# Kernel optimization log

Hardware: AMD Instinct MI355X
Metric: run time of the kernel (lower is better)

The kernel has to match this reference:

```python
import jax, jax.numpy as jnp
from jax import lax
import numpy as np

B, T, D, H = 64, 512, 1024, 1024

def _lstm_layer(x_tbd, mask_tb, W, U, b):
    """Keras-style LSTM over time-major x (T,B,D). Gate order i,f,g,o.
    Masked timesteps carry previous h,c (Keras mask semantics)."""
    Bsz = x_tbd.shape[1]
    Hsz = U.shape[0]
    # precompute input projection once: (T,B,4H)
    xz = jnp.einsum('tbd,dh->tbh', x_tbd, W) + b

    def step(carry, inp):
        h, c = carry
        zx, m = inp
        z = zx + h @ U
        i, f, g, o = jnp.split(z, 4, axis=-1)
        i = jax.nn.sigmoid(i)
        f = jax.nn.sigmoid(f)
        g = jnp.tanh(g)
        o = jax.nn.sigmoid(o)
        c_new = f * c + i * g
        h_new = o * jnp.tanh(c_new)
        m = m[:, None]
        h2 = jnp.where(m, h_new, h)
        c2 = jnp.where(m, c_new, c)
        return (h2, c2), h2

    h0 = jnp.zeros((Bsz, Hsz), x_tbd.dtype)
    c0 = jnp.zeros((Bsz, Hsz), x_tbd.dtype)
    (h, c), hs = lax.scan(step, (h0, c0), (xz, mask_tb))
    return hs, h, c


def setup_inputs() -> dict:
    key = jax.random.key(0)
    ks = jax.random.split(key, 8)
    sD = 1.0 / np.sqrt(D)
    sH = 1.0 / np.sqrt(H)
    x = jax.random.normal(ks[0], (B, T, D), dtype=jnp.float32)
    lengths = jax.random.randint(ks[1], (B,), 1, T + 1, dtype=jnp.int32)
    # Keras unit_forget_bias: bias zeros except forget gate slice = 1
    b = jnp.zeros((4 * H,), jnp.float32).at[H:2 * H].set(1.0)
    return {
        'x': x,
        'lengths': lengths,
        'W0': jax.random.normal(ks[2], (D, 4 * H), dtype=jnp.float32) * sD,
        'U0': jax.random.normal(ks[3], (H, 4 * H), dtype=jnp.float32) * sH,
        'b0': b,
        'W1': jax.random.normal(ks[4], (H, 4 * H), dtype=jnp.float32) * sH,
        'U1': jax.random.normal(ks[5], (H, 4 * H), dtype=jnp.float32) * sH,
        'b1': b,
    }


def reference(x, lengths, W0, U0, b0, W1, U1, b1):
    Tlen = x.shape[1]
    mask = jnp.arange(Tlen)[None, :] < lengths[:, None]  # (B,T)
    mask_tb = mask.T  # (T,B)
    x_tbd = jnp.transpose(x, (1, 0, 2))  # time-major
    out0, _, _ = _lstm_layer(x_tbd, mask_tb, W0, U0, b0)
    out1, h, c = _lstm_layer(out0, mask_tb, W1, U1, b1)
    rnnout = jnp.transpose(out1, (1, 0, 2))  # (B,T,H)
    return rnnout, h, c
```

## Files before the change

kernel.cpp:

```cpp
#include <hip/hip_runtime.h>
#include <hip/hip_bf16.h>


#define NTT 512

typedef __attribute__((ext_vector_type(8))) short short8;
typedef __attribute__((ext_vector_type(4))) float floatx4;
typedef __attribute__((ext_vector_type(4))) unsigned short ushort4v;
typedef unsigned long long ull;

#define LDS_TOTAL 90112

#define AT_LD(p) __hip_atomic_load((p), __ATOMIC_RELAXED, __HIP_MEMORY_SCOPE_AGENT)
#define AT_ST(p, v) __hip_atomic_store((p), (v), __ATOMIC_RELAXED, __HIP_MEMORY_SCOPE_AGENT)
#define AT_ADD(p, v) __hip_atomic_fetch_add((p), (v), __ATOMIC_RELAXED, __HIP_MEMORY_SCOPE_AGENT)

__device__ __forceinline__ unsigned short f2bf(float f) {
  unsigned int u = __float_as_uint(f);
  u += 0x7fffu + ((u >> 16) & 1u);
  return (unsigned short)(u >> 16);
}
__device__ __forceinline__ float sigmf(float x) { return 1.0f / (1.0f + __expf(-x)); }
__device__ __forceinline__ float tanhfa(float x) { return 1.0f - 2.0f / (1.0f + __expf(2.0f * x)); }

__device__ __forceinline__ void fullbar(ull* fb) {
  __syncthreads();
  if (threadIdx.x == 0) {
    __builtin_amdgcn_fence(__ATOMIC_RELEASE, "agent");
    AT_ADD(fb, 1ull);
    while (AT_LD(fb) < 256ull) __builtin_amdgcn_s_sleep(1);
    __builtin_amdgcn_fence(__ATOMIC_ACQUIRE, "agent");
  }
  __syncthreads();
}

__device__ __forceinline__ void layer_arrive(ull* base, int sub) {
  asm volatile("s_waitcnt vmcnt(0)" ::: "memory");
  __syncthreads();
  if (threadIdx.x == 0) AT_ADD(base + 16 + 16 * (sub & 7), 1ull);
}

__device__ __forceinline__ ull leafmin(const ull* base) {
  ull v[8];
#pragma unroll
  for (int l = 0; l < 8; ++l) v[l] = AT_LD(base + 16 + 16 * l);
  ull m = v[0];
#pragma unroll
  for (int l = 1; l < 8; ++l) m = v[l] < m ? v[l] : m;
  return m;
}

__device__ __forceinline__ void wait2(const ull* own, long long ot, const ull* oth, long long xt) {
  if (threadIdx.x == 0) {
    if (ot > 0) {
      const ull tgt = 16ull * (ull)ot;
      while (leafmin(own) < tgt) __builtin_amdgcn_s_sleep(1);
    }
    if (xt > 0) {
      const ull tgt = 16ull * (ull)xt;
      while (leafmin(oth) < tgt) __builtin_amdgcn_s_sleep(1);
    }
    __builtin_amdgcn_fence(__ATOMIC_ACQUIRE, "agent");
  }
  __syncthreads();
}

__device__ __forceinline__ short8 ldfrag(const char* p) { return *(const short8*)p; }

__device__ __forceinline__ void ringfill(const char* const* aPm, short8 (*af)[4]) {
#pragma unroll
  for (int kt = 0; kt < 8; ++kt)
#pragma unroll
    for (int mt = 0; mt < 4; ++mt) af[kt][mt] = ldfrag(aPm[mt] + kt * 64);
}

__device__ __forceinline__ void kmain(const char* const* aPm, short8 (*af)[4],
                                      const short8 (*bfr)[2], floatx4 (*acc)[2]) {
#pragma unroll
  for (int kt = 0; kt < 16; ++kt) {
#pragma unroll
    for (int mt = 0; mt < 4; ++mt)
#pragma unroll
      for (int nt = 0; nt < 2; ++nt)
        acc[mt][nt] = __builtin_amdgcn_mfma_f32_16x16x32_bf16(
            af[kt & 7][mt], bfr[kt][nt], acc[mt][nt], 0, 0, 0);
    if (kt < 8) {
#pragma unroll
      for (int mt = 0; mt < 4; ++mt)
        af[kt & 7][mt] = ldfrag(aPm[mt] + (kt + 8) * 64);
    }
  }
}

__global__ __launch_bounds__(256, 1) void lstm2_persist(
    const float* __restrict__ xin, const int* __restrict__ lens,
    const float* __restrict__ W0, const float* __restrict__ U0, const float* __restrict__ b0v,
    const float* __restrict__ W1, const float* __restrict__ U1, const float* __restrict__ b1v,
    float* __restrict__ out, ull* __restrict__ ws) {
  extern __shared__ char smem[];
  float* red = (float*)smem;

  ull* bar0 = ws;
  ull* bar1 = ws + 512;
  ull* fbar = ws + 1024;
  unsigned short* hbufs = (unsigned short*)(ws + 2048);

  const int tid = threadIdx.x;
  const int bid = blockIdx.x;
  const int layer = bid >> 7;
  const int sub = bid & 127;
  const int hc0 = sub * 8;
  const int wave = tid >> 6;
  const int lane = tid & 63;
  const int c16 = lane & 15;
  const int rowgrp = lane >> 4;

  unsigned short* h0r[4] = {hbufs, hbufs + 65536, hbufs + 131072, hbufs + 196608};
  unsigned short* h1r[2] = {hbufs + 262144, hbufs + 327680};

  const unsigned int gid = (unsigned int)bid * 256u + (unsigned int)tid;
  for (unsigned int i = gid; i < 196608u; i += 65536u) ((unsigned int*)hbufs)[i] = 0u;
  {
    const floatx4* xs = (const floatx4*)xin;
    for (unsigned int q = gid; q < 8388608u; q += 65536u) {
      unsigned int d4 = q & 255u;
      unsigned int bt = q >> 8;
      floatx4 v = xs[q];
      ushort4v o;
      o.x = f2bf(v.x); o.y = f2bf(v.y); o.z = f2bf(v.z); o.w = f2bf(v.w);
      *((ushort4v*)((char*)out + (size_t)bt * 4096) + d4) = o;
    }
  }
  const float* Wm = layer ? W1 : W0;
  const float* Um = layer ? U1 : U0;
  const float* Bsrc = (wave < 2) ? Wm : Um;
  const int kbase = (wave & 1) * 512;
  short8 bf[16][2];
#pragma unroll
  for (int kt = 0; kt < 16; ++kt)
#pragma unroll
    for (int nt = 0; nt < 2; ++nt) {
      const int zc = (nt * 2 + (c16 >> 3)) * 1024 + hc0 + (c16 & 7);
      const float* col = Bsrc + (size_t)(kbase + kt * 32 + rowgrp * 8) * 4096 + zc;
      short8 v;
#pragma unroll
      for (int j = 0; j < 8; ++j) v[j] = (short)f2bf(col[(size_t)j * 4096]);
      bf[kt][nt] = v;
    }
  const float* bv = layer ? b1v : b0v;
  const float bias0 = bv[(c16 >> 3) * 1024 + hc0 + (c16 & 7)];
  const float bias1 = bv[(2 + (c16 >> 3)) * 1024 + hc0 + (c16 & 7)];
  int lens4[4];
#pragma unroll
  for (int r = 0; r < 4; ++r) lens4[r] = lens[wave * 16 + rowgrp * 4 + r];

  fullbar(fbar);

  float hst[4] = {0.f, 0.f, 0.f, 0.f};
  float cst[4] = {0.f, 0.f, 0.f, 0.f};
  const int col = hc0 + c16;

#pragma unroll 1
  for (int t = 0; t < NTT; ++t) {
    const char* aPm[4];
    short8 af[8][4];
    bool isX;
    {
      const char* base0;
      size_t pitch;
      if (layer == 0) {
        if (wave < 2) { base0 = (const char*)out + (size_t)t * 4096 + (size_t)wave * 1024;
                        pitch = (size_t)NTT * 4096; isX = true; }
        else          { base0 = (const char*)h0r[(t + 3) & 3] + (size_t)(wave - 2) * 1024;
                        pitch = 2048; isX = false; }
      } else {
        if (wave < 2) { base0 = (const char*)h0r[t & 3] + (size_t)wave * 1024; }
        else          { base0 = (const char*)h1r[(t + 1) & 1] + (size_t)(wave - 2) * 1024; }
        pitch = 2048; isX = false;
      }
      const char* aP = base0 + (size_t)c16 * pitch + (size_t)rowgrp * 16;
#pragma unroll
      for (int mt = 0; mt < 4; ++mt) aPm[mt] = aP + (size_t)mt * 16 * pitch;
    }

    if (isX) ringfill(aPm, af);

    if (layer == 0) wait2(bar0, t, bar1, (long long)t - 3);
    else            wait2(bar1, t, bar0, (long long)t + 1);

    floatx4 acc[4][2];
#pragma unroll
    for (int mt = 0; mt < 4; ++mt)
#pragma unroll
      for (int nt = 0; nt < 2; ++nt) { floatx4 z = {0.f, 0.f, 0.f, 0.f}; acc[mt][nt] = z; }

    if (isX) {
      kmain(aPm, af, bf, acc);
    } else {
      ringfill(aPm, af);
      kmain(aPm, af, bf, acc);
    }

#pragma unroll
    for (int mt = 0; mt < 4; ++mt)
      if (mt != wave) {
        int slot = mt * 3 + wave - (wave > mt ? 1 : 0);
        *(floatx4*)&red[((slot * 2 + 0) * 64 + lane) * 4] = acc[mt][0];
        *(floatx4*)&red[((slot * 2 + 1) * 64 + lane) * 4] = acc[mt][1];
      }
    __syncthreads();
    floatx4 z0 = acc[wave][0], z1 = acc[wave][1];
#pragma unroll
    for (int q = 0; q < 3; ++q) {
      int slot = wave * 3 + q;
      z0 += *(const floatx4*)&red[((slot * 2 + 0) * 64 + lane) * 4];
      z1 += *(const floatx4*)&red[((slot * 2 + 1) * 64 + lane) * 4];
    }
    z0 += bias0;
    z1 += bias1;

    unsigned short* hW = layer ? h1r[t & 1] : h0r[t & 3];
    float2 f2s[4];

#pragma unroll
    for (int r = 0; r < 4; ++r) {
      float zi = z0[r], zg = z1[r];
      float zf = __shfl_xor(zi, 8);
      float zo = __shfl_xor(zg, 8);
      float h2, hu_f = 0.f;
      unsigned short hu = 0;
      if (c16 < 8) {
        float ig = sigmf(zi), fg = sigmf(zf), gg = tanhfa(zg), og = sigmf(zo);
        float cn = fg * cst[r] + ig * gg;
        float hn = og * tanhfa(cn);
        bool m = t < lens4[r];
        h2 = m ? hn : hst[r];
        float c2 = m ? cn : cst[r];
        hst[r] = h2;
        cst[r] = c2;
        hu = f2bf(h2);
        hu_f = h2;
      }
      unsigned int up = __shfl_xor((unsigned int)hu, 1);
      float hp = __shfl_xor(hu_f, 1);
      if (c16 < 8 && !(c16 & 1)) {
        int b = wave * 16 + rowgrp * 4 + r;
        unsigned int w = (unsigned int)hu | (up << 16);
        AT_ST((unsigned int*)(hW + b * 1024 + col), w);
        f2s[r] = make_float2(hu_f, hp);
      }
    }

    if (layer == 0) layer_arrive(bar0, sub);
    else            layer_arrive(bar1, sub);

    if (layer && c16 < 8 && !(c16 & 1)) {
#pragma unroll
      for (int r = 0; r < 4; ++r) {
        int b = wave * 16 + rowgrp * 4 + r;
        *(float2*)&out[((size_t)b * 512 + (size_t)t) * 1024 + col] = f2s[r];
      }
    }
  }

  if (layer && c16 < 8) {
#pragma unroll
    for (int r = 0; r < 4; ++r) {
      int b = wave * 16 + rowgrp * 4 + r;
      out[(size_t)33554432 + (size_t)b * 1024 + col] = hst[r];
      out[(size_t)33554432 + 65536 + (size_t)b * 1024 + col] = cst[r];
    }
  }
}

extern "C" void kernel_launch(void* const* d_in, const int* in_sizes, int n_in,
                              void* d_out, int out_size, void* d_ws, size_t ws_size,
                              hipStream_t stream) {
  (void)in_sizes; (void)n_in; (void)out_size; (void)ws_size;
  const float* x  = (const float*)d_in[0];
  const int* lens = (const int*)d_in[1];
  const float* W0 = (const float*)d_in[2];
  const float* U0 = (const float*)d_in[3];
  const float* b0 = (const float*)d_in[4];
  const float* W1 = (const float*)d_in[5];
  const float* U1 = (const float*)d_in[6];
  const float* b1 = (const float*)d_in[7];

  (void)hipFuncSetAttribute((const void*)lstm2_persist,
                            hipFuncAttributeMaxDynamicSharedMemorySize, LDS_TOTAL);
  hipMemsetAsync(d_ws, 0, 16384, stream);

  lstm2_persist<<<dim3(256), dim3(256), LDS_TOTAL, stream>>>(
      x, lens, W0, U0, b0, W1, U1, b1, (float*)d_out, (ull*)d_ws);
}
```

Measured before the change: 9.748 ms.

## Halve persistent grid to 128 blocks, each computing 16 hidden columns

The persistent two-layer LSTM kernel now launches 128 blocks instead of 256, with each block owning 16 hidden units instead of 8. That doubles the register-resident weight fragments and the MFMA accumulators per block, and the A-fragment ring is shrunk from 8 to 4 k-steps to make room. The aim is to halve the number of participants in the per-timestep cross-block barriers and reuse each loaded h/x fragment across twice as many MFMAs. The costs are higher register pressure (possible spills), twice the serial MFMA work per block on each step, and only half of the CUs in use.

```diff
diff --git a/kernel.cpp b/kernel.cpp
--- a/kernel.cpp
+++ b/kernel.cpp
@@ -28,7 +28,7 @@
   if (threadIdx.x == 0) {
     __builtin_amdgcn_fence(__ATOMIC_RELEASE, "agent");
     AT_ADD(fb, 1ull);
-    while (AT_LD(fb) < 256ull) __builtin_amdgcn_s_sleep(1);
+    while (AT_LD(fb) < 128ull) __builtin_amdgcn_s_sleep(1);
     __builtin_amdgcn_fence(__ATOMIC_ACQUIRE, "agent");
   }
   __syncthreads();
@@ -53,11 +53,11 @@
 __device__ __forceinline__ void wait2(const ull* own, long long ot, const ull* oth, long long xt) {
   if (threadIdx.x == 0) {
     if (ot > 0) {
-      const ull tgt = 16ull * (ull)ot;
+      const ull tgt = 8ull * (ull)ot;
       while (leafmin(own) < tgt) __builtin_amdgcn_s_sleep(1);
     }
     if (xt > 0) {
-      const ull tgt = 16ull * (ull)xt;
+      const ull tgt = 8ull * (ull)xt;
       while (leafmin(oth) < tgt) __builtin_amdgcn_s_sleep(1);
     }
     __builtin_amdgcn_fence(__ATOMIC_ACQUIRE, "agent");
@@ -69,25 +69,25 @@
 
 __device__ __forceinline__ void ringfill(const char* const* aPm, short8 (*af)[4]) {
 #pragma unroll
-  for (int kt = 0; kt < 8; ++kt)
+  for (int kt = 0; kt < 4; ++kt)
 #pragma unroll
     for (int mt = 0; mt < 4; ++mt) af[kt][mt] = ldfrag(aPm[mt] + kt * 64);
 }
 
 __device__ __forceinline__ void kmain(const char* const* aPm, short8 (*af)[4],
-                                      const short8 (*bfr)[2], floatx4 (*acc)[2]) {
+                                      const short8 (*bfr)[4], floatx4 (*acc)[4]) {
 #pragma unroll
   for (int kt = 0; kt < 16; ++kt) {
 #pragma unroll
     for (int mt = 0; mt < 4; ++mt)
 #pragma unroll
-      for (int nt = 0; nt < 2; ++nt)
+      for (int nt = 0; nt < 4; ++nt)
         acc[mt][nt] = __builtin_amdgcn_mfma_f32_16x16x32_bf16(
-            af[kt & 7][mt], bfr[kt][nt], acc[mt][nt], 0, 0, 0);
-    if (kt < 8) {
+            af[kt & 3][mt], bfr[kt][nt], acc[mt][nt], 0, 0, 0);
+    if (kt < 12) {
 #pragma unroll
       for (int mt = 0; mt < 4; ++mt)
-        af[kt & 7][mt] = ldfrag(aPm[mt] + (kt + 8) * 64);
+        af[kt & 3][mt] = ldfrag(aPm[mt] + (kt + 4) * 64);
     }
   }
 }
@@ -107,9 +107,9 @@
 
   const int tid = threadIdx.x;
   const int bid = blockIdx.x;
-  const int layer = bid >> 7;
-  const int sub = bid & 127;
-  const int hc0 = sub * 8;
+  const int layer = bid >> 6;
+  const int sub = bid & 63;
+  const int hc0 = sub * 16;
   const int wave = tid >> 6;
   const int lane = tid & 63;
   const int c16 = lane & 15;
@@ -119,10 +119,10 @@
   unsigned short* h1r[2] = {hbufs + 262144, hbufs + 327680};
 
   const unsigned int gid = (unsigned int)bid * 256u + (unsigned int)tid;
-  for (unsigned int i = gid; i < 196608u; i += 65536u) ((unsigned int*)hbufs)[i] = 0u;
+  for (unsigned int i = gid; i < 196608u; i += 32768u) ((unsigned int*)hbufs)[i] = 0u;
   {
     const floatx4* xs = (const floatx4*)xin;
-    for (unsigned int q = gid; q < 8388608u; q += 65536u) {
+    for (unsigned int q = gid; q < 8388608u; q += 32768u) {
       unsigned int d4 = q & 255u;
       unsigned int bt = q >> 8;
       floatx4 v = xs[q];
@@ -135,12 +135,12 @@
   const float* Um = layer ? U1 : U0;
   const float* Bsrc = (wave < 2) ? Wm : Um;
   const int kbase = (wave & 1) * 512;
-  short8 bf[16][2];
+  short8 bf[16][4];
 #pragma unroll
   for (int kt = 0; kt < 16; ++kt)
 #pragma unroll
-    for (int nt = 0; nt < 2; ++nt) {
-      const int zc = (nt * 2 + (c16 >> 3)) * 1024 + hc0 + (c16 & 7);
+    for (int nt = 0; nt < 4; ++nt) {
+      const int zc = ((nt & 1) * 2 + (c16 >> 3)) * 1024 + hc0 + (nt >> 1) * 8 + (c16 & 7);
       const float* col = Bsrc + (size_t)(kbase + kt * 32 + rowgrp * 8) * 4096 + zc;
       short8 v;
 #pragma unroll
@@ -148,22 +148,25 @@
       bf[kt][nt] = v;
     }
   const float* bv = layer ? b1v : b0v;
-  const float bias0 = bv[(c16 >> 3) * 1024 + hc0 + (c16 & 7)];
-  const float bias1 = bv[(2 + (c16 >> 3)) * 1024 + hc0 + (c16 & 7)];
+  float bias0[2], bias1[2];
+#pragma unroll
+  for (int ch = 0; ch < 2; ++ch) {
+    bias0[ch] = bv[(c16 >> 3) * 1024 + hc0 + ch * 8 + (c16 & 7)];
+    bias1[ch] = bv[(2 + (c16 >> 3)) * 1024 + hc0 + ch * 8 + (c16 & 7)];
+  }
   int lens4[4];
 #pragma unroll
   for (int r = 0; r < 4; ++r) lens4[r] = lens[wave * 16 + rowgrp * 4 + r];
 
   fullbar(fbar);
 
-  float hst[4] = {0.f, 0.f, 0.f, 0.f};
-  float cst[4] = {0.f, 0.f, 0.f, 0.f};
-  const int col = hc0 + c16;
+  float hst[2][4] = {{0.f, 0.f, 0.f, 0.f}, {0.f, 0.f, 0.f, 0.f}};
+  float cst[2][4] = {{0.f, 0.f, 0.f, 0.f}, {0.f, 0.f, 0.f, 0.f}};
 
 #pragma unroll 1
   for (int t = 0; t < NTT; ++t) {
     const char* aPm[4];
-    short8 af[8][4];
+    short8 af[4][4];
     bool isX;
     {
       const char* base0;
@@ -188,11 +191,11 @@
     if (layer == 0) wait2(bar0, t, bar1, (long long)t - 3);
     else            wait2(bar1, t, bar0, (long long)t + 1);
 
-    floatx4 acc[4][2];
+    floatx4 acc[4][4];
 #pragma unroll
     for (int mt = 0; mt < 4; ++mt)
 #pragma unroll
-      for (int nt = 0; nt < 2; ++nt) { floatx4 z = {0.f, 0.f, 0.f, 0.f}; acc[mt][nt] = z; }
+      for (int nt = 0; nt < 4; ++nt) { floatx4 z = {0.f, 0.f, 0.f, 0.f}; acc[mt][nt] = z; }
 
     if (isX) {
       kmain(aPm, af, bf, acc);
@@ -205,49 +208,60 @@
     for (int mt = 0; mt < 4; ++mt)
       if (mt != wave) {
         int slot = mt * 3 + wave - (wave > mt ? 1 : 0);
-        *(floatx4*)&red[((slot * 2 + 0) * 64 + lane) * 4] = acc[mt][0];
-        *(floatx4*)&red[((slot * 2 + 1) * 64 + lane) * 4] = acc[mt][1];
+#pragma unroll
+        for (int nt = 0; nt < 4; ++nt)
+          *(floatx4*)&red[((slot * 4 + nt) * 64 + lane) * 4] = acc[mt][nt];
       }
     __syncthreads();
-    floatx4 z0 = acc[wave][0], z1 = acc[wave][1];
+    floatx4 z[4];
+#pragma unroll
+    for (int nt = 0; nt < 4; ++nt) z[nt] = acc[wave][nt];
 #pragma unroll
     for (int q = 0; q < 3; ++q) {
       int slot = wave * 3 + q;
-      z0 += *(const floatx4*)&red[((slot * 2 + 0) * 64 + lane) * 4];
-      z1 += *(const floatx4*)&red[((slot * 2 + 1) * 64 + lane) * 4];
-    }
-    z0 += bias0;
-    z1 += bias1;
+#pragma unroll
+      for (int nt = 0; nt < 4; ++nt)
+        z[nt] += *(const floatx4*)&red[((slot * 4 + nt) * 64 + lane) * 4];
+    }
+#pragma unroll
+    for (int ch = 0; ch < 2; ++ch) {
+      z[ch * 2 + 0] += bias0[ch];
+      z[ch * 2 + 1] += bias1[ch];
+    }
 
     unsigned short* hW = layer ? h1r[t & 1] : h0r[t & 3];
-    float2 f2s[4];
-
-#pragma unroll
-    for (int r = 0; r < 4; ++r) {
-      float zi = z0[r], zg = z1[r];
-      float zf = __shfl_xor(zi, 8);
-      float zo = __shfl_xor(zg, 8);
-      float h2, hu_f = 0.f;
-      unsigned short hu = 0;
-      if (c16 < 8) {
-        float ig = sigmf(zi), fg = sigmf(zf), gg = tanhfa(zg), og = sigmf(zo);
-        float cn = fg * cst[r] + ig * gg;
-        float hn = og * tanhfa(cn);
-        bool m = t < lens4[r];
-        h2 = m ? hn : hst[r];
-        float c2 = m ? cn : cst[r];
-        hst[r] = h2;
-        cst[r] = c2;
-        hu = f2bf(h2);
-        hu_f = h2;
-      }
-      unsigned int up = __shfl_xor((unsigned int)hu, 1);
-      float hp = __shfl_xor(hu_f, 1);
-      if (c16 < 8 && !(c16 & 1)) {
-        int b = wave * 16 + rowgrp * 4 + r;
-        unsigned int w = (unsigned int)hu | (up << 16);
-        AT_ST((unsigned int*)(hW + b * 1024 + col), w);
-        f2s[r] = make_float2(hu_f, hp);
+    float2 f2s[2][4];
+
+#pragma unroll
+    for (int ch = 0; ch < 2; ++ch) {
+      const int col = hc0 + ch * 8 + c16;
+#pragma unroll
+      for (int r = 0; r < 4; ++r) {
+        float zi = z[ch * 2 + 0][r], zg = z[ch * 2 + 1][r];
+        float zf = __shfl_xor(zi, 8);
+        float zo = __shfl_xor(zg, 8);
+        float h2, hu_f = 0.f;
+        unsigned short hu = 0;
+        if (c16 < 8) {
+          float ig = sigmf(zi), fg = sigmf(zf), gg = tanhfa(zg), og = sigmf(zo);
+          float cn = fg * cst[ch][r] + ig * gg;
+          float hn = og * tanhfa(cn);
+          bool m = t < lens4[r];
+          h2 = m ? hn : hst[ch][r];
+          float c2 = m ? cn : cst[ch][r];
+          hst[ch][r] = h2;
+          cst[ch][r] = c2;
+          hu = f2bf(h2);
+          hu_f = h2;
+        }
+        unsigned int up = __shfl_xor((unsigned int)hu, 1);
+        float hp = __shfl_xor(hu_f, 1);
+        if (c16 < 8 && !(c16 & 1)) {
+          int b = wave * 16 + rowgrp * 4 + r;
+          unsigned int w = (unsigned int)hu | (up << 16);
+          AT_ST((unsigned int*)(hW + b * 1024 + col), w);
+          f2s[ch][r] = make_float2(hu_f, hp);
+        }
       }
     }
 
@@ -256,19 +270,27 @@
 
     if (layer && c16 < 8 && !(c16 & 1)) {
 #pragma unroll
+      for (int ch = 0; ch < 2; ++ch) {
+        const int col = hc0 + ch * 8 + c16;
+#pragma unroll
+        for (int r = 0; r < 4; ++r) {
+          int b = wave * 16 + rowgrp * 4 + r;
+          *(float2*)&out[((size_t)b * 512 + (size_t)t) * 1024 + col] = f2s[ch][r];
+        }
+      }
+    }
+  }
+
+  if (layer && c16 < 8) {
+#pragma unroll
+    for (int ch = 0; ch < 2; ++ch) {
+      const int col = hc0 + ch * 8 + c16;
+#pragma unroll
       for (int r = 0; r < 4; ++r) {
         int b = wave * 16 + rowgrp * 4 + r;
-        *(float2*)&out[((size_t)b * 512 + (size_t)t) * 1024 + col] = f2s[r];
-      }
-    }
-  }
-
-  if (layer && c16 < 8) {
-#pragma unroll
-    for (int r = 0; r < 4; ++r) {
-      int b = wave * 16 + rowgrp * 4 + r;
-      out[(size_t)33554432 + (size_t)b * 1024 + col] = hst[r];
-      out[(size_t)33554432 + 65536 + (size_t)b * 1024 + col] = cst[r];
+        out[(size_t)33554432 + (size_t)b * 1024 + col] = hst[ch][r];
+        out[(size_t)33554432 + 65536 + (size_t)b * 1024 + col] = cst[ch][r];
+      }
     }
   }
 }
@@ -290,6 +312,6 @@
                             hipFuncAttributeMaxDynamicSharedMemorySize, LDS_TOTAL);
   hipMemsetAsync(d_ws, 0, 16384, stream);
 
-  lstm2_persist<<<dim3(256), dim3(256), LDS_TOTAL, stream>>>(
+  lstm2_persist<<<dim3(128), dim3(256), LDS_TOTAL, stream>>>(
       x, lens, W0, U0, b0, W1, U1, b1, (float*)d_out, (ull*)d_ws);
 }
```

Result: slower. 21.41 ms (+119.6%).

## Replace tree-counter barriers with per-block step flags and chunked waits

Applied to the files above, without the earlier changes.

Replaces the leaf-counter barrier (atomic adds plus a min over 8 leaves, waited on by thread 0 and then a block sync) with one flag word per producer block holding its latest timestep. Each wave polls only the 64 producer flags for the h slice it reads, using ballot. It then loads and computes in 4-chunk K slices as soon as each group of 16 producers is ready, overlapping the MFMA work with late producers. This cuts barrier latency and serialization on the recurrent critical path. The cost is more polling traffic, and the wait now relies on per-flag release ordering: there is no explicit acquire fence, only relaxed atomic loads.

```diff
diff --git a/kernel.cpp b/kernel.cpp
--- a/kernel.cpp
+++ b/kernel.cpp
@@ -34,38 +34,13 @@
   __syncthreads();
 }
 
-__device__ __forceinline__ void layer_arrive(ull* base, int sub) {
-  asm volatile("s_waitcnt vmcnt(0)" ::: "memory");
-  __syncthreads();
-  if (threadIdx.x == 0) AT_ADD(base + 16 + 16 * (sub & 7), 1ull);
-}
-
-__device__ __forceinline__ ull leafmin(const ull* base) {
-  ull v[8];
-#pragma unroll
-  for (int l = 0; l < 8; ++l) v[l] = AT_LD(base + 16 + 16 * l);
-  ull m = v[0];
-#pragma unroll
-  for (int l = 1; l < 8; ++l) m = v[l] < m ? v[l] : m;
-  return m;
-}
-
-__device__ __forceinline__ void wait2(const ull* own, long long ot, const ull* oth, long long xt) {
-  if (threadIdx.x == 0) {
-    if (ot > 0) {
-      const ull tgt = 16ull * (ull)ot;
-      while (leafmin(own) < tgt) __builtin_amdgcn_s_sleep(1);
-    }
-    if (xt > 0) {
-      const ull tgt = 16ull * (ull)xt;
-      while (leafmin(oth) < tgt) __builtin_amdgcn_s_sleep(1);
-    }
-    __builtin_amdgcn_fence(__ATOMIC_ACQUIRE, "agent");
-  }
-  __syncthreads();
-}
-
 __device__ __forceinline__ short8 ldfrag(const char* p) { return *(const short8*)p; }
+__device__ __forceinline__ short8 ldcoh(const char* p) {
+  union { short8 s; ull q[2]; } u;
+  u.q[0] = AT_LD((const ull*)p);
+  u.q[1] = AT_LD((const ull*)(p + 8));
+  return u.s;
+}
 
 __device__ __forceinline__ void ringfill(const char* const* aPm, short8 (*af)[4]) {
 #pragma unroll
@@ -90,6 +65,25 @@
         af[kt & 7][mt] = ldfrag(aPm[mt] + (kt + 8) * 64);
     }
   }
+}
+
+__device__ __forceinline__ void ringchunk(const char* const* aPm, short8 (*afc)[4], int kb) {
+#pragma unroll
+  for (int j = 0; j < 4; ++j)
+#pragma unroll
+    for (int mt = 0; mt < 4; ++mt) afc[j][mt] = ldcoh(aPm[mt] + (kb + j) * 64);
+}
+
+__device__ __forceinline__ void kchunk(const short8 (*afc)[4], const short8 (*bfr)[2],
+                                       floatx4 (*acc)[2], int kb) {
+#pragma unroll
+  for (int j = 0; j < 4; ++j)
+#pragma unroll
+    for (int mt = 0; mt < 4; ++mt)
+#pragma unroll
+      for (int nt = 0; nt < 2; ++nt)
+        acc[mt][nt] = __builtin_amdgcn_mfma_f32_16x16x32_bf16(
+            afc[j][mt], bfr[kb + j][nt], acc[mt][nt], 0, 0, 0);
 }
 
 __global__ __launch_bounds__(256, 1) void lstm2_persist(
@@ -100,8 +94,8 @@
   extern __shared__ char smem[];
   float* red = (float*)smem;
 
-  ull* bar0 = ws;
-  ull* bar1 = ws + 512;
+  unsigned* flags0 = (unsigned*)(ws + 16);
+  unsigned* flags1 = (unsigned*)(ws + 80);
   ull* fbar = ws + 1024;
   unsigned short* hbufs = (unsigned short*)(ws + 2048);
 
@@ -114,6 +108,7 @@
   const int lane = tid & 63;
   const int c16 = lane & 15;
   const int rowgrp = lane >> 4;
+  unsigned* flagsL = layer ? flags1 : flags0;
 
   unsigned short* h0r[4] = {hbufs, hbufs + 65536, hbufs + 131072, hbufs + 196608};
   unsigned short* h1r[2] = {hbufs + 262144, hbufs + 327680};
@@ -183,11 +178,6 @@
       for (int mt = 0; mt < 4; ++mt) aPm[mt] = aP + (size_t)mt * 16 * pitch;
     }
 
-    if (isX) ringfill(aPm, af);
-
-    if (layer == 0) wait2(bar0, t, bar1, (long long)t - 3);
-    else            wait2(bar1, t, bar0, (long long)t + 1);
-
     floatx4 acc[4][2];
 #pragma unroll
     for (int mt = 0; mt < 4; ++mt)
@@ -195,10 +185,37 @@
       for (int nt = 0; nt < 2; ++nt) { floatx4 z = {0.f, 0.f, 0.f, 0.f}; acc[mt][nt] = z; }
 
     if (isX) {
+      ringfill(aPm, af);
       kmain(aPm, af, bf, acc);
     } else {
-      ringfill(aPm, af);
-      kmain(aPm, af, bf, acc);
+      if (layer == 0 && t >= 4) {
+        const unsigned g4 = (unsigned)(t - 3);
+        while (true) {
+          bool ok = (AT_LD(flags1 + lane) >= g4) && (AT_LD(flags1 + 64 + lane) >= g4);
+          if (__all(ok)) break;
+          __builtin_amdgcn_s_sleep(2);
+        }
+      }
+      const unsigned* fl;
+      int half;
+      unsigned tgt;
+      if (layer == 0)      { fl = flags0; half = wave - 2; tgt = (unsigned)t; }
+      else if (wave < 2)   { fl = flags0; half = wave;     tgt = (unsigned)(t + 1); }
+      else                 { fl = flags1; half = wave - 2; tgt = (unsigned)t; }
+      const unsigned* fb = fl + half * 64;
+
+      ull rdy = __ballot(AT_LD(fb + lane) >= tgt);
+#pragma unroll
+      for (int g = 0; g < 4; ++g) {
+        const ull need = 0xFFFFull << (16 * g);
+        while ((rdy & need) != need) {
+          __builtin_amdgcn_s_sleep(1);
+          rdy = __ballot(AT_LD(fb + lane) >= tgt);
+        }
+        ringchunk(aPm, &af[(g & 1) * 4], g * 4);
+        if (g) kchunk(&af[((g - 1) & 1) * 4], bf, acc, (g - 1) * 4);
+      }
+      kchunk(&af[4], bf, acc, 12);
     }
 
 #pragma unroll
@@ -251,8 +268,9 @@
       }
     }
 
-    if (layer == 0) layer_arrive(bar0, sub);
-    else            layer_arrive(bar1, sub);
+    asm volatile("s_waitcnt vmcnt(0)" ::: "memory");
+    __syncthreads();
+    if (tid == 0) AT_ST(flagsL + sub, (unsigned)(t + 1));
 
     if (layer && c16 < 8 && !(c16 & 1)) {
 #pragma unroll
```

After: 10.23 ms. 4.9% more time.
